# Kernel tuning notes

Measured on AMD Instinct MI355X. Metric: run time of the kernel, lower is better.

## Reference

```python
import jax, jax.numpy as jnp
import numpy as np

N = 100_000   # nodes
E = 1_600_000 # edges
D = 128       # hidden/input dim
OUT = 32      # output dim
G = 512       # graphs in batch
L = 3         # conv layers


def setup_inputs() -> dict:
    key = jax.random.key(0)
    ks = jax.random.split(key, 12)
    s = 1.0 / np.sqrt(D)
    inp = {
        "x": jax.random.normal(ks[0], (N, D), jnp.float32),
        "edge_index": jax.random.randint(ks[1], (2, E), 0, N, dtype=jnp.int32),
        "batch": jnp.sort(jax.random.randint(ks[2], (N,), 0, G, dtype=jnp.int32)),
        "enc_W1": jax.random.normal(ks[3], (D, D), jnp.float32) * s,
        "enc_b1": jnp.zeros((D,), jnp.float32),
        "enc_W2": jax.random.normal(ks[4], (D, D), jnp.float32) * s,
        "enc_b2": jnp.zeros((D,), jnp.float32),
        "gcn_W": jax.random.normal(ks[5], (L, D, D), jnp.float32) * s,
        "gcn_b": jnp.zeros((L, D), jnp.float32),
        "dec_W1": jax.random.normal(ks[6], (D, D), jnp.float32) * s,
        "dec_b1": jnp.zeros((D,), jnp.float32),
        "dec_W2": jax.random.normal(ks[7], (D, OUT), jnp.float32) * s,
        "dec_b2": jnp.zeros((OUT,), jnp.float32),
        "num_graphs": G,
    }
    return inp


def reference(x, edge_index, batch, enc_W1, enc_b1, enc_W2, enc_b2,
              gcn_W, gcn_b, dec_W1, dec_b1, dec_W2, dec_b2, num_graphs):
    n = x.shape[0]
    src, dst = edge_index[0], edge_index[1]

    # ---- encoder MLP (Linear -> ReLU -> Linear -> ReLU) ----
    h = jax.nn.relu(x @ enc_W1 + enc_b1)
    h = jax.nn.relu(h @ enc_W2 + enc_b2)

    # ---- GCN normalization: D^{-1/2} (A + I) D^{-1/2}, degrees incl. self-loops ----
    deg = jax.ops.segment_sum(jnp.ones_like(src, dtype=h.dtype), dst, num_segments=n) + 1.0
    inv_sqrt = jax.lax.rsqrt(deg)           # [N]
    edge_coef = inv_sqrt[src] * inv_sqrt[dst]  # [E]
    self_coef = inv_sqrt * inv_sqrt            # [N]

    # ---- GCN conv layers ----
    for l in range(gcn_W.shape[0]):
        hw = h @ gcn_W[l]                                       # [N, D]
        msgs = hw[src] * edge_coef[:, None]                     # [E, D] gather
        agg = jax.ops.segment_sum(msgs, dst, num_segments=n)    # [N, D] scatter-add
        agg = agg + hw * self_coef[:, None]                     # self loops
        h = jax.nn.relu(agg + gcn_b[l])

    # ---- global add pool over graphs ----
    pooled = jax.ops.segment_sum(h, batch, num_segments=num_graphs)  # [G, D]

    # ---- decoder MLP ----
    out = jax.nn.relu(pooled @ dec_W1 + dec_b1)
    return out @ dec_W2 + dec_b2
```

## Files before the change

kernel.cpp:

```cpp
#include <hip/hip_runtime.h>

#define NNODES 100000
#define NEDGES 1600000
#define DIM    128
#define OUTD   32
#define NGRAPH 512
#define LDA    136

#define NBUCK2  256
#define BSHIFT  9
#define CAP     12288
#define EPB2    8192
#define SBLOCKS ((NEDGES + EPB2 - 1) / EPB2)
#define NBUILD  ((NNODES + 511) / 512)
#define FBLOCKS ((NNODES + 127) / 128)

using bf16x8 = __attribute__((ext_vector_type(8))) short;
using f32x4  = __attribute__((ext_vector_type(4))) float;
using f32x2  = __attribute__((ext_vector_type(2))) float;

__device__ __forceinline__ short f2bf(float f) {
    unsigned u = __float_as_uint(f);
    unsigned r = (u + 0x7fff + ((u >> 16) & 1)) >> 16;
    return (short)r;
}
__device__ __forceinline__ float bf2f(short s) {
    return __uint_as_float(((unsigned)(unsigned short)s) << 16);
}
__device__ __forceinline__ float bf2f_lo(unsigned u) { return __uint_as_float(u << 16); }
__device__ __forceinline__ float bf2f_hi(unsigned u) { return __uint_as_float(u & 0xffff0000u); }

__device__ __forceinline__ uint2 bf8_to_fp8(bf16x8 t) {
    float f0 = bf2f(t[0]), f1 = bf2f(t[1]), f2 = bf2f(t[2]), f3 = bf2f(t[3]);
    float f4 = bf2f(t[4]), f5 = bf2f(t[5]), f6 = bf2f(t[6]), f7 = bf2f(t[7]);
    uint2 o;
    o.x = __builtin_amdgcn_cvt_pk_fp8_f32(f0, f1, 0, false);
    o.x = __builtin_amdgcn_cvt_pk_fp8_f32(f2, f3, o.x, true);
    o.y = __builtin_amdgcn_cvt_pk_fp8_f32(f4, f5, 0, false);
    o.y = __builtin_amdgcn_cvt_pk_fp8_f32(f6, f7, o.y, true);
    return o;
}

__global__ __launch_bounds__(256) void k_prep(
    const float* __restrict__ eW1, const float* __restrict__ eW2,
    const float* __restrict__ gW, short* __restrict__ WT,
    int* __restrict__ gcur, float* __restrict__ pooled)
{
    int idx = blockIdx.x * 256 + threadIdx.x;
    if (idx < 5 * 16384) {
        int mat = idx >> 14, rem = idx & 16383;
        int k = rem >> 7, n = rem & 127;
        const float* src = (mat == 0) ? eW1 : (mat == 1) ? eW2
                                            : (gW + (size_t)(mat - 2) * 16384);
        WT[(size_t)mat * 16384 + n * DIM + k] = f2bf(src[k * DIM + n]);
    }
    if (idx < NBUCK2) gcur[idx] = idx * CAP;
    if (idx < NGRAPH * DIM) pooled[idx] = 0.f;
}

__global__ __launch_bounds__(512) void k_scatter(
    const int* __restrict__ src, const int* __restrict__ dst,
    int* __restrict__ gcur, unsigned* __restrict__ tmp)
{
    __shared__ unsigned short rnk[EPB2];
    __shared__ int h[NBUCK2];
    __shared__ int gbase[NBUCK2];
    const int tid  = threadIdx.x;
    const int base = blockIdx.x * EPB2;
    if (tid < NBUCK2) h[tid] = 0;
    __syncthreads();
    #pragma unroll
    for (int it = 0; it < EPB2 / 512; ++it) {
        int e = base + it * 512 + tid;
        if (e < NEDGES) {
            int b = dst[e] >> BSHIFT;
            rnk[it * 512 + tid] = (unsigned short)atomicAdd(&h[b], 1);
        }
    }
    __syncthreads();
    if (tid < NBUCK2 && h[tid] > 0)
        gbase[tid] = atomicAdd(&gcur[tid], h[tid]);
    __syncthreads();
    #pragma unroll
    for (int it = 0; it < EPB2 / 512; ++it) {
        int e = base + it * 512 + tid;
        if (e < NEDGES) {
            int d = dst[e], sv = src[e];
            int b = d >> BSHIFT;
            int pos = gbase[b] + rnk[it * 512 + tid];
            if (pos < (b + 1) * CAP)
                tmp[pos] = (unsigned)sv | ((unsigned)(d & 511) << 17);
        }
    }
}

__global__ __launch_bounds__(512) void k_build(
    const unsigned* __restrict__ tmp, const int* __restrict__ gcur,
    int* __restrict__ row_off, int* __restrict__ cntA,
    float* __restrict__ inv, int* __restrict__ col)
{
    __shared__ int hist[512], sc[512], lcur[512];
    const int tid   = threadIdx.x;
    const int b     = blockIdx.x;
    const int tbase = b * CAP;
    const int cnt_b = min(gcur[b] - tbase, CAP);
    hist[tid] = 0;
    __syncthreads();
    for (int i = tid; i < cnt_b; i += 512)
        atomicAdd(&hist[(tmp[tbase + i] >> 17) & 511], 1);
    __syncthreads();
    const int hv = hist[tid];
    sc[tid] = hv;
    __syncthreads();
    for (int off = 1; off < 512; off <<= 1) {
        int t = (tid >= off) ? sc[tid - off] : 0;
        __syncthreads();
        sc[tid] += t;
        __syncthreads();
    }
    const int start = tbase + sc[tid] - hv;
    lcur[tid] = start;
    const int node = b * 512 + tid;
    if (node < NNODES) {
        row_off[node] = start;
        cntA[node]    = hv;
        inv[node]     = rsqrtf((float)hv + 1.0f);
    }
    __syncthreads();
    for (int i = tid; i < cnt_b; i += 512) {
        unsigned t = tmp[tbase + i];
        int pos = atomicAdd(&lcur[(t >> 17) & 511], 1);
        col[pos] = (int)(t & 0x1FFFFu);
    }
}

__global__ __launch_bounds__(512, 4) void k_enc(
    const float* __restrict__ x, const short* __restrict__ WT,
    const float* __restrict__ b1, const float* __restrict__ b2,
    const float* __restrict__ inv, unsigned char* __restrict__ g8, int M)
{
    __shared__ short As[128 * LDA];
    __shared__ short Bs[128 * LDA];

    const int tid = threadIdx.x;
    const int m0  = blockIdx.x * 128;

    #pragma unroll
    for (int i = 0; i < 4; ++i) {
        int u = tid + i * 512;
        int row = u >> 4, uc = (u & 15) << 3;
        int gr = min(m0 + row, M - 1);
        const float4* sp = (const float4*)(x + (size_t)gr * DIM + uc);
        float4 f0 = sp[0], f1 = sp[1];
        short t8[8] = { f2bf(f0.x), f2bf(f0.y), f2bf(f0.z), f2bf(f0.w),
                        f2bf(f1.x), f2bf(f1.y), f2bf(f1.z), f2bf(f1.w) };
        *(bf16x8*)&As[row * LDA + uc] = *(bf16x8*)t8;
    }

    const int wave = tid >> 6, lane = tid & 63;
    const int ml = lane & 15, quad = lane >> 4;
    const int w16 = wave * 16;

    #pragma unroll
    for (int mat = 0; mat < 3; ++mat) {
        if (mat > 0) __syncthreads();
        #pragma unroll
        for (int i = 0; i < 4; ++i) {
            int u = tid + i * 512;
            int n = u >> 4, kc = (u & 15) << 3;
            *(bf16x8*)&Bs[n * LDA + kc] =
                *(const bf16x8*)(WT + (size_t)mat * 16384 + n * DIM + kc);
        }
        __syncthreads();

        f32x4 acc[8] = {};
        #pragma unroll
        for (int kk = 0; kk < 4; ++kk) {
            const int k0 = kk * 32 + quad * 8;
            bf16x8 a = *(bf16x8*)&As[(w16 + ml) * LDA + k0];
            #pragma unroll
            for (int ni = 0; ni < 8; ++ni) {
                bf16x8 b = *(bf16x8*)&Bs[(ni * 16 + ml) * LDA + k0];
                acc[ni] = __builtin_amdgcn_mfma_f32_16x16x32_bf16(a, b, acc[ni], 0, 0, 0);
            }
        }
        #pragma unroll
        for (int ni = 0; ni < 8; ++ni) {
            const int colc = ni * 16 + ml;
            #pragma unroll
            for (int r = 0; r < 4; ++r) {
                const int rowl = w16 + quad * 4 + r;
                float v = acc[ni][r];
                if (mat == 0)      v = fmaxf(v + b1[colc], 0.f);
                else if (mat == 1) v = fmaxf(v + b2[colc], 0.f);
                else               v *= inv[min(m0 + rowl, M - 1)];
                As[rowl * LDA + colc] = f2bf(v);
            }
        }
    }
    __syncthreads();

    #pragma unroll
    for (int i = 0; i < 4; ++i) {
        int u = tid + i * 512;
        int row = u >> 4, uc = (u & 15) << 3;
        int gr = m0 + row;
        if (gr < M) {
            bf16x8 t = *(bf16x8*)&As[row * LDA + uc];
            *(uint2*)(g8 + (size_t)gr * DIM + uc) = bf8_to_fp8(t);
        }
    }
}

__global__ __launch_bounds__(256) void gemm_mfma(
    const short* __restrict__ A, const short* __restrict__ WT,
    const float* __restrict__ inv, unsigned char* __restrict__ g8, int M)
{
    __shared__ short As[128 * LDA];
    __shared__ short Bs[128 * LDA];

    const int tid = threadIdx.x;
    const int m0  = blockIdx.x * 128;

    #pragma unroll
    for (int i = 0; i < 8; ++i) {
        int idx = tid + i * 256;
        int row = idx >> 4, kg = (idx & 15) << 3;
        int r = min(m0 + row, M - 1);
        *(bf16x8*)&As[row * LDA + kg] = *(const bf16x8*)(A + (size_t)r * DIM + kg);
    }
    #pragma unroll
    for (int i = 0; i < 8; ++i) {
        int idx = tid + i * 256;
        int n = idx >> 4, kg = (idx & 15) << 3;
        *(bf16x8*)&Bs[n * LDA + kg] = *(const bf16x8*)(WT + n * DIM + kg);
    }
    __syncthreads();

    const int wave = tid >> 6, lane = tid & 63;
    const int ml = lane & 15, quad = lane >> 4;
    const int w32 = wave * 32;

    f32x4 acc[2][8] = {};
    #pragma unroll
    for (int kk = 0; kk < 4; ++kk) {
        const int k0 = kk * 32 + quad * 8;
        bf16x8 a0 = *(bf16x8*)&As[(w32 + ml) * LDA + k0];
        bf16x8 a1 = *(bf16x8*)&As[(w32 + 16 + ml) * LDA + k0];
        #pragma unroll
        for (int ni = 0; ni < 8; ++ni) {
            bf16x8 b = *(bf16x8*)&Bs[(ni * 16 + ml) * LDA + k0];
            acc[0][ni] = __builtin_amdgcn_mfma_f32_16x16x32_bf16(a0, b, acc[0][ni], 0, 0, 0);
            acc[1][ni] = __builtin_amdgcn_mfma_f32_16x16x32_bf16(a1, b, acc[1][ni], 0, 0, 0);
        }
    }
    __syncthreads();

    short* Cs = As;
    #pragma unroll
    for (int mi = 0; mi < 2; ++mi) {
        #pragma unroll
        for (int ni = 0; ni < 8; ++ni) {
            const int colc = ni * 16 + ml;
            #pragma unroll
            for (int r = 0; r < 4; ++r) {
                const int row = w32 + mi * 16 + quad * 4 + r;
                float v = acc[mi][ni][r] * inv[min(m0 + row, M - 1)];
                Cs[row * LDA + colc] = f2bf(v);
            }
        }
    }
    __syncthreads();
    #pragma unroll
    for (int i = 0; i < 8; ++i) {
        int idx = tid + i * 256;
        int row = idx >> 4, cg = (idx & 15) << 3;
        int gr = m0 + row;
        if (gr < M) {
            bf16x8 t = *(bf16x8*)&Cs[row * LDA + cg];
            *(uint2*)(g8 + (size_t)gr * DIM + cg) = bf8_to_fp8(t);
        }
    }
}

__global__ __launch_bounds__(512) void k_agg(
    const unsigned char* __restrict__ g8v, const int* __restrict__ row_off,
    const int* __restrict__ cntA, const int* __restrict__ col,
    const float* __restrict__ inv, const float* __restrict__ bias,
    short* __restrict__ hout)
{
    const int wid  = blockIdx.x * 8 + (threadIdx.x >> 6);
    const int lane = threadIdx.x & 63;
    const int q    = lane >> 4;
    const int sl   = lane & 15;
    const int node = wid * 4 + q;
    if (node >= NNODES) return;

    const uint2* hp = (const uint2*)g8v;
    uint2 us = hp[(size_t)node * 16 + sl];
    f32x2 p;
    float a0, a1, a2, a3, a4, a5, a6, a7;
    p = __builtin_amdgcn_cvt_pk_f32_fp8(us.x, false); a0 = p.x; a1 = p.y;
    p = __builtin_amdgcn_cvt_pk_f32_fp8(us.x, true);  a2 = p.x; a3 = p.y;
    p = __builtin_amdgcn_cvt_pk_f32_fp8(us.y, false); a4 = p.x; a5 = p.y;
    p = __builtin_amdgcn_cvt_pk_f32_fp8(us.y, true);  a6 = p.x; a7 = p.y;

    #define ACC8(v) \
        p = __builtin_amdgcn_cvt_pk_f32_fp8(v.x, false); a0 += p.x; a1 += p.y; \
        p = __builtin_amdgcn_cvt_pk_f32_fp8(v.x, true);  a2 += p.x; a3 += p.y; \
        p = __builtin_amdgcn_cvt_pk_f32_fp8(v.y, false); a4 += p.x; a5 += p.y; \
        p = __builtin_amdgcn_cvt_pk_f32_fp8(v.y, true);  a6 += p.x; a7 += p.y;

    const int s = row_off[node];
    const int e = s + cntA[node];
    int j = s;
    for (; j + 7 < e; j += 8) {
        uint2 v0 = hp[(size_t)col[j]     * 16 + sl];
        uint2 v1 = hp[(size_t)col[j + 1] * 16 + sl];
        uint2 v2 = hp[(size_t)col[j + 2] * 16 + sl];
        uint2 v3 = hp[(size_t)col[j + 3] * 16 + sl];
        uint2 v4 = hp[(size_t)col[j + 4] * 16 + sl];
        uint2 v5 = hp[(size_t)col[j + 5] * 16 + sl];
        uint2 v6 = hp[(size_t)col[j + 6] * 16 + sl];
        uint2 v7 = hp[(size_t)col[j + 7] * 16 + sl];
        ACC8(v0) ACC8(v1) ACC8(v2) ACC8(v3)
        ACC8(v4) ACC8(v5) ACC8(v6) ACC8(v7)
    }
    for (; j + 3 < e; j += 4) {
        uint2 v0 = hp[(size_t)col[j]     * 16 + sl];
        uint2 v1 = hp[(size_t)col[j + 1] * 16 + sl];
        uint2 v2 = hp[(size_t)col[j + 2] * 16 + sl];
        uint2 v3 = hp[(size_t)col[j + 3] * 16 + sl];
        ACC8(v0) ACC8(v1) ACC8(v2) ACC8(v3)
    }
    for (; j < e; ++j) {
        uint2 v = hp[(size_t)col[j] * 16 + sl];
        ACC8(v)
    }
    #undef ACC8

    const float scv = inv[node];
    const float4 bb0 = ((const float4*)bias)[sl * 2];
    const float4 bb1 = ((const float4*)bias)[sl * 2 + 1];
    short o[8];
    o[0] = f2bf(fmaxf(fmaf(a0, scv, bb0.x), 0.f));
    o[1] = f2bf(fmaxf(fmaf(a1, scv, bb0.y), 0.f));
    o[2] = f2bf(fmaxf(fmaf(a2, scv, bb0.z), 0.f));
    o[3] = f2bf(fmaxf(fmaf(a3, scv, bb0.w), 0.f));
    o[4] = f2bf(fmaxf(fmaf(a4, scv, bb1.x), 0.f));
    o[5] = f2bf(fmaxf(fmaf(a5, scv, bb1.y), 0.f));
    o[6] = f2bf(fmaxf(fmaf(a6, scv, bb1.z), 0.f));
    o[7] = f2bf(fmaxf(fmaf(a7, scv, bb1.w), 0.f));
    ((bf16x8*)hout)[(size_t)node * 16 + sl] = *(bf16x8*)o;
}

__global__ __launch_bounds__(512) void k_pool(
    const short* __restrict__ h, const int* __restrict__ batch,
    float* __restrict__ pooled)
{
    const int wave = threadIdx.x >> 6, lane = threadIdx.x & 63;
    const int node0 = blockIdx.x * 128 + wave * 16;
    const unsigned* hp = (const unsigned*)h;

    float gx = 0.f, gy = 0.f;
    int cg = -1;
    #pragma unroll 1
    for (int i = 0; i < 16; ++i) {
        const int node = node0 + i;
        if (node >= NNODES) break;
        const int g = batch[node];
        if (g != cg) {
            if (cg >= 0) {
                atomicAdd(pooled + (size_t)cg * DIM + lane * 2,     gx);
                atomicAdd(pooled + (size_t)cg * DIM + lane * 2 + 1, gy);
            }
            cg = g; gx = 0.f; gy = 0.f;
        }
        unsigned v = hp[(size_t)node * 64 + lane];
        gx += bf2f_lo(v);
        gy += bf2f_hi(v);
    }
    if (cg >= 0) {
        atomicAdd(pooled + (size_t)cg * DIM + lane * 2,     gx);
        atomicAdd(pooled + (size_t)cg * DIM + lane * 2 + 1, gy);
    }
}

__global__ __launch_bounds__(512) void k_dec(
    const float* __restrict__ pooled, const float* __restrict__ W1,
    const float* __restrict__ b1, const float* __restrict__ W2,
    const float* __restrict__ b2, float* __restrict__ out)
{
    __shared__ float pbuf[8][128];
    __shared__ float tbuf[8][128];
    const int wave = threadIdx.x >> 6, lane = threadIdx.x & 63;
    const int g = blockIdx.x * 8 + wave;

    float2 pv = *(const float2*)(pooled + (size_t)g * DIM + lane * 2);
    pbuf[wave][lane * 2]     = pv.x;
    pbuf[wave][lane * 2 + 1] = pv.y;
    __syncthreads();

    float t0 = 0.f, t1 = 0.f;
    #pragma unroll 8
    for (int k = 0; k < DIM; ++k) {
        float pk = pbuf[wave][k];
        float2 w = *(const float2*)(W1 + (size_t)k * DIM + lane * 2);
        t0 = fmaf(pk, w.x, t0);
        t1 = fmaf(pk, w.y, t1);
    }
    tbuf[wave][lane * 2]     = fmaxf(t0 + b1[lane * 2],     0.f);
    tbuf[wave][lane * 2 + 1] = fmaxf(t1 + b1[lane * 2 + 1], 0.f);
    __syncthreads();

    const int c = lane & 31, hh = lane >> 5;
    float part = 0.f;
    #pragma unroll 8
    for (int kk = 0; kk < 64; ++kk) {
        int k = hh * 64 + kk;
        part = fmaf(tbuf[wave][k], W2[(size_t)k * OUTD + c], part);
    }
    float other = __shfl_xor(part, 32, 64);
    if (hh == 0)
        out[(size_t)g * OUTD + c] = part + other + b2[c];
}

extern "C" void kernel_launch(void* const* d_in, const int* in_sizes, int n_in,
                              void* d_out, int out_size, void* d_ws, size_t ws_size,
                              hipStream_t stream)
{
    const float* x      = (const float*)d_in[0];
    const int*   ei     = (const int*)d_in[1];
    const int*   batch  = (const int*)d_in[2];
    const float* enc_W1 = (const float*)d_in[3];
    const float* enc_b1 = (const float*)d_in[4];
    const float* enc_W2 = (const float*)d_in[5];
    const float* enc_b2 = (const float*)d_in[6];
    const float* gcn_W  = (const float*)d_in[7];
    const float* gcn_b  = (const float*)d_in[8];
    const float* dec_W1 = (const float*)d_in[9];
    const float* dec_b1 = (const float*)d_in[10];
    const float* dec_W2 = (const float*)d_in[11];
    const float* dec_b2 = (const float*)d_in[12];
    float* out = (float*)d_out;

    const int* src = ei;
    const int* dst = ei + NEDGES;

    char* p = (char*)d_ws;
    auto alloc = [&](size_t bytes) -> void* {
        void* r = (void*)p;
        p += (bytes + 255) & ~(size_t)255;
        return r;
    };
    short*         hw     = (short*)        alloc((size_t)NNODES * DIM * sizeof(short));
    unsigned char* g8     = (unsigned char*)alloc((size_t)NNODES * DIM);
    float*         inv    = (float*)        alloc((size_t)NNODES * sizeof(float));
    int*           row_off= (int*)          alloc((size_t)NNODES * sizeof(int));
    int*           cntA   = (int*)          alloc((size_t)NNODES * sizeof(int));
    int*           col    = (int*)          alloc((size_t)NBUCK2 * CAP * sizeof(int));
    unsigned*      tmp    = (unsigned*)     alloc((size_t)NBUCK2 * CAP * sizeof(unsigned));
    int*           gcur   = (int*)          alloc((size_t)NBUCK2 * sizeof(int));
    short*         WT     = (short*)        alloc((size_t)5 * DIM * DIM * sizeof(short));
    float*         pooled = (float*)        alloc((size_t)NGRAPH * DIM * sizeof(float));

    k_prep   <<<(5 * 16384 + 255) / 256, 256, 0, stream>>>(enc_W1, enc_W2, gcn_W,
                                                           WT, gcur, pooled);
    k_scatter<<<SBLOCKS, 512, 0, stream>>>(src, dst, gcur, tmp);
    k_build  <<<NBUILD, 512, 0, stream>>>(tmp, gcur, row_off, cntA, inv, col);

    k_enc<<<FBLOCKS, 512, 0, stream>>>(x, WT, enc_b1, enc_b2, inv, g8, NNODES);

    const int aggBlocks = (NNODES + 31) / 32;
    k_agg<<<aggBlocks, 512, 0, stream>>>(g8, row_off, cntA, col, inv, gcn_b, hw);
    gemm_mfma<<<FBLOCKS, 256, 0, stream>>>(hw, WT + 3 * 16384, inv, g8, NNODES);
    k_agg<<<aggBlocks, 512, 0, stream>>>(g8, row_off, cntA, col, inv, gcn_b + 128, hw);
    gemm_mfma<<<FBLOCKS, 256, 0, stream>>>(hw, WT + 4 * 16384, inv, g8, NNODES);
    k_agg<<<aggBlocks, 512, 0, stream>>>(g8, row_off, cntA, col, inv, gcn_b + 256, hw);

    k_pool<<<FBLOCKS, 512, 0, stream>>>(hw, batch, pooled);
    k_dec <<<NGRAPH / 8, 512, 0, stream>>>(pooled, dec_W1, dec_b1,
                                           dec_W2, dec_b2, out);
}
```

Measured before the change: 334.9 us.

## Fuse GCN aggregation with next-layer GEMM and final aggregation with pooling

Aggregation for layers one and two now runs its MFMA transform to the next layer in the same kernel, with a 32-row tile per block. The bf16 hidden-state round trip through global memory and the separate GEMM launches are gone, and two fp8 buffers are ping-ponged. The last aggregation now sums into the graph pooling through shared memory, which replaces the separate pool kernel. In exchange each aggregation block reloads the full 128x128 weight tile, and the small per-block GEMM gives the MFMA units less work per wave.

```diff
diff --git a/kernel.cpp b/kernel.cpp
--- a/kernel.cpp
+++ b/kernel.cpp
@@ -14,6 +14,7 @@
 #define SBLOCKS ((NEDGES + EPB2 - 1) / EPB2)
 #define NBUILD  ((NNODES + 511) / 512)
 #define FBLOCKS ((NNODES + 127) / 128)
+#define AGGBLK  ((NNODES + 31) / 32)
 
 using bf16x8 = __attribute__((ext_vector_type(8))) short;
 using f32x4  = __attribute__((ext_vector_type(4))) float;
@@ -27,8 +28,6 @@
 __device__ __forceinline__ float bf2f(short s) {
     return __uint_as_float(((unsigned)(unsigned short)s) << 16);
 }
-__device__ __forceinline__ float bf2f_lo(unsigned u) { return __uint_as_float(u << 16); }
-__device__ __forceinline__ float bf2f_hi(unsigned u) { return __uint_as_float(u & 0xffff0000u); }
 
 __device__ __forceinline__ uint2 bf8_to_fp8(bf16x8 t) {
     float f0 = bf2f(t[0]), f1 = bf2f(t[1]), f2 = bf2f(t[2]), f3 = bf2f(t[3]);
@@ -212,89 +211,30 @@
     }
 }
 
-__global__ __launch_bounds__(256) void gemm_mfma(
-    const short* __restrict__ A, const short* __restrict__ WT,
-    const float* __restrict__ inv, unsigned char* __restrict__ g8, int M)
-{
-    __shared__ short As[128 * LDA];
-    __shared__ short Bs[128 * LDA];
-
-    const int tid = threadIdx.x;
-    const int m0  = blockIdx.x * 128;
-
-    #pragma unroll
-    for (int i = 0; i < 8; ++i) {
-        int idx = tid + i * 256;
-        int row = idx >> 4, kg = (idx & 15) << 3;
-        int r = min(m0 + row, M - 1);
-        *(bf16x8*)&As[row * LDA + kg] = *(const bf16x8*)(A + (size_t)r * DIM + kg);
-    }
-    #pragma unroll
-    for (int i = 0; i < 8; ++i) {
-        int idx = tid + i * 256;
-        int n = idx >> 4, kg = (idx & 15) << 3;
-        *(bf16x8*)&Bs[n * LDA + kg] = *(const bf16x8*)(WT + n * DIM + kg);
-    }
-    __syncthreads();
-
-    const int wave = tid >> 6, lane = tid & 63;
-    const int ml = lane & 15, quad = lane >> 4;
-    const int w32 = wave * 32;
-
-    f32x4 acc[2][8] = {};
-    #pragma unroll
-    for (int kk = 0; kk < 4; ++kk) {
-        const int k0 = kk * 32 + quad * 8;
-        bf16x8 a0 = *(bf16x8*)&As[(w32 + ml) * LDA + k0];
-        bf16x8 a1 = *(bf16x8*)&As[(w32 + 16 + ml) * LDA + k0];
-        #pragma unroll
-        for (int ni = 0; ni < 8; ++ni) {
-            bf16x8 b = *(bf16x8*)&Bs[(ni * 16 + ml) * LDA + k0];
-            acc[0][ni] = __builtin_amdgcn_mfma_f32_16x16x32_bf16(a0, b, acc[0][ni], 0, 0, 0);
-            acc[1][ni] = __builtin_amdgcn_mfma_f32_16x16x32_bf16(a1, b, acc[1][ni], 0, 0, 0);
-        }
-    }
-    __syncthreads();
-
-    short* Cs = As;
-    #pragma unroll
-    for (int mi = 0; mi < 2; ++mi) {
-        #pragma unroll
-        for (int ni = 0; ni < 8; ++ni) {
-            const int colc = ni * 16 + ml;
-            #pragma unroll
-            for (int r = 0; r < 4; ++r) {
-                const int row = w32 + mi * 16 + quad * 4 + r;
-                float v = acc[mi][ni][r] * inv[min(m0 + row, M - 1)];
-                Cs[row * LDA + colc] = f2bf(v);
-            }
-        }
-    }
-    __syncthreads();
-    #pragma unroll
-    for (int i = 0; i < 8; ++i) {
-        int idx = tid + i * 256;
-        int row = idx >> 4, cg = (idx & 15) << 3;
-        int gr = m0 + row;
-        if (gr < M) {
-            bf16x8 t = *(bf16x8*)&Cs[row * LDA + cg];
-            *(uint2*)(g8 + (size_t)gr * DIM + cg) = bf8_to_fp8(t);
-        }
-    }
-}
-
-__global__ __launch_bounds__(512) void k_agg(
+__global__ __launch_bounds__(512) void k_agg_gemm(
     const unsigned char* __restrict__ g8v, const int* __restrict__ row_off,
     const int* __restrict__ cntA, const int* __restrict__ col,
     const float* __restrict__ inv, const float* __restrict__ bias,
-    short* __restrict__ hout)
-{
-    const int wid  = blockIdx.x * 8 + (threadIdx.x >> 6);
-    const int lane = threadIdx.x & 63;
+    const short* __restrict__ WT, unsigned char* __restrict__ g8o)
+{
+    __shared__ short As[32 * LDA];
+    __shared__ short Bs[128 * LDA];
+
+    const int tid = threadIdx.x;
+
+    #pragma unroll
+    for (int i = 0; i < 4; ++i) {
+        int u = tid + i * 512;
+        int n = u >> 4, kc = (u & 15) << 3;
+        *(bf16x8*)&Bs[n * LDA + kc] = *(const bf16x8*)(WT + n * DIM + kc);
+    }
+
+    const int wave = tid >> 6, lane = tid & 63;
     const int q    = lane >> 4;
     const int sl   = lane & 15;
-    const int node = wid * 4 + q;
-    if (node >= NNODES) return;
+    const int nl   = wave * 4 + q;
+    const int m0   = blockIdx.x * 32;
+    const int node = m0 + nl;
 
     const uint2* hp = (const uint2*)g8v;
     uint2 us = hp[(size_t)node * 16 + sl];
@@ -351,39 +291,135 @@
     o[5] = f2bf(fmaxf(fmaf(a5, scv, bb1.y), 0.f));
     o[6] = f2bf(fmaxf(fmaf(a6, scv, bb1.z), 0.f));
     o[7] = f2bf(fmaxf(fmaf(a7, scv, bb1.w), 0.f));
-    ((bf16x8*)hout)[(size_t)node * 16 + sl] = *(bf16x8*)o;
-}
-
-__global__ __launch_bounds__(512) void k_pool(
-    const short* __restrict__ h, const int* __restrict__ batch,
-    float* __restrict__ pooled)
-{
-    const int wave = threadIdx.x >> 6, lane = threadIdx.x & 63;
-    const int node0 = blockIdx.x * 128 + wave * 16;
-    const unsigned* hp = (const unsigned*)h;
-
-    float gx = 0.f, gy = 0.f;
+    *(bf16x8*)&As[nl * LDA + sl * 8] = *(bf16x8*)o;
+    __syncthreads();
+
+    const int mh = wave >> 2;
+    const int nq = wave & 3;
+    f32x4 acc[2] = {};
+    #pragma unroll
+    for (int kk = 0; kk < 4; ++kk) {
+        const int k0 = kk * 32 + q * 8;
+        bf16x8 a = *(bf16x8*)&As[(mh * 16 + sl) * LDA + k0];
+        #pragma unroll
+        for (int ni = 0; ni < 2; ++ni) {
+            bf16x8 b = *(bf16x8*)&Bs[((nq * 2 + ni) * 16 + sl) * LDA + k0];
+            acc[ni] = __builtin_amdgcn_mfma_f32_16x16x32_bf16(a, b, acc[ni], 0, 0, 0);
+        }
+    }
+    __syncthreads();
+
+    #pragma unroll
+    for (int ni = 0; ni < 2; ++ni) {
+        const int colc = (nq * 2 + ni) * 16 + sl;
+        #pragma unroll
+        for (int r = 0; r < 4; ++r) {
+            const int rowl = mh * 16 + q * 4 + r;
+            As[rowl * LDA + colc] = f2bf(acc[ni][r] * inv[m0 + rowl]);
+        }
+    }
+    __syncthreads();
+
+    {
+        int row = tid >> 4, cg = (tid & 15) << 3;
+        bf16x8 t = *(bf16x8*)&As[row * LDA + cg];
+        *(uint2*)(g8o + (size_t)(m0 + row) * DIM + cg) = bf8_to_fp8(t);
+    }
+}
+
+__global__ __launch_bounds__(512) void k_agg_pool(
+    const unsigned char* __restrict__ g8v, const int* __restrict__ row_off,
+    const int* __restrict__ cntA, const int* __restrict__ col,
+    const float* __restrict__ inv, const float* __restrict__ bias,
+    const int* __restrict__ batch, float* __restrict__ pooled)
+{
+    __shared__ float Hs[32][132];
+    __shared__ int sbatch[32];
+
+    const int tid = threadIdx.x;
+    const int wave = tid >> 6, lane = tid & 63;
+    const int q    = lane >> 4;
+    const int sl   = lane & 15;
+    const int nl   = wave * 4 + q;
+    const int m0   = blockIdx.x * 32;
+    const int node = m0 + nl;
+
+    if (tid < 32) sbatch[tid] = batch[m0 + tid];
+
+    const uint2* hp = (const uint2*)g8v;
+    uint2 us = hp[(size_t)node * 16 + sl];
+    f32x2 p;
+    float a0, a1, a2, a3, a4, a5, a6, a7;
+    p = __builtin_amdgcn_cvt_pk_f32_fp8(us.x, false); a0 = p.x; a1 = p.y;
+    p = __builtin_amdgcn_cvt_pk_f32_fp8(us.x, true);  a2 = p.x; a3 = p.y;
+    p = __builtin_amdgcn_cvt_pk_f32_fp8(us.y, false); a4 = p.x; a5 = p.y;
+    p = __builtin_amdgcn_cvt_pk_f32_fp8(us.y, true);  a6 = p.x; a7 = p.y;
+
+    #define ACC8(v) \
+        p = __builtin_amdgcn_cvt_pk_f32_fp8(v.x, false); a0 += p.x; a1 += p.y; \
+        p = __builtin_amdgcn_cvt_pk_f32_fp8(v.x, true);  a2 += p.x; a3 += p.y; \
+        p = __builtin_amdgcn_cvt_pk_f32_fp8(v.y, false); a4 += p.x; a5 += p.y; \
+        p = __builtin_amdgcn_cvt_pk_f32_fp8(v.y, true);  a6 += p.x; a7 += p.y;
+
+    const int s = row_off[node];
+    const int e = s + cntA[node];
+    int j = s;
+    for (; j + 7 < e; j += 8) {
+        uint2 v0 = hp[(size_t)col[j]     * 16 + sl];
+        uint2 v1 = hp[(size_t)col[j + 1] * 16 + sl];
+        uint2 v2 = hp[(size_t)col[j + 2] * 16 + sl];
+        uint2 v3 = hp[(size_t)col[j + 3] * 16 + sl];
+        uint2 v4 = hp[(size_t)col[j + 4] * 16 + sl];
+        uint2 v5 = hp[(size_t)col[j + 5] * 16 + sl];
+        uint2 v6 = hp[(size_t)col[j + 6] * 16 + sl];
+        uint2 v7 = hp[(size_t)col[j + 7] * 16 + sl];
+        ACC8(v0) ACC8(v1) ACC8(v2) ACC8(v3)
+        ACC8(v4) ACC8(v5) ACC8(v6) ACC8(v7)
+    }
+    for (; j + 3 < e; j += 4) {
+        uint2 v0 = hp[(size_t)col[j]     * 16 + sl];
+        uint2 v1 = hp[(size_t)col[j + 1] * 16 + sl];
+        uint2 v2 = hp[(size_t)col[j + 2] * 16 + sl];
+        uint2 v3 = hp[(size_t)col[j + 3] * 16 + sl];
+        ACC8(v0) ACC8(v1) ACC8(v2) ACC8(v3)
+    }
+    for (; j < e; ++j) {
+        uint2 v = hp[(size_t)col[j] * 16 + sl];
+        ACC8(v)
+    }
+    #undef ACC8
+
+    const float scv = inv[node];
+    const float4 bb0 = ((const float4*)bias)[sl * 2];
+    const float4 bb1 = ((const float4*)bias)[sl * 2 + 1];
+    float4 h0, h1;
+    h0.x = fmaxf(fmaf(a0, scv, bb0.x), 0.f);
+    h0.y = fmaxf(fmaf(a1, scv, bb0.y), 0.f);
+    h0.z = fmaxf(fmaf(a2, scv, bb0.z), 0.f);
+    h0.w = fmaxf(fmaf(a3, scv, bb0.w), 0.f);
+    h1.x = fmaxf(fmaf(a4, scv, bb1.x), 0.f);
+    h1.y = fmaxf(fmaf(a5, scv, bb1.y), 0.f);
+    h1.z = fmaxf(fmaf(a6, scv, bb1.z), 0.f);
+    h1.w = fmaxf(fmaf(a7, scv, bb1.w), 0.f);
+    *(float4*)&Hs[nl][sl * 8]     = h0;
+    *(float4*)&Hs[nl][sl * 8 + 4] = h1;
+    __syncthreads();
+
+    const int d   = tid & 127;
+    const int grp = tid >> 7;
+    float acc = 0.f;
     int cg = -1;
-    #pragma unroll 1
-    for (int i = 0; i < 16; ++i) {
-        const int node = node0 + i;
-        if (node >= NNODES) break;
-        const int g = batch[node];
+    #pragma unroll
+    for (int i = 0; i < 8; ++i) {
+        const int nn = grp * 8 + i;
+        const int g  = sbatch[nn];
         if (g != cg) {
-            if (cg >= 0) {
-                atomicAdd(pooled + (size_t)cg * DIM + lane * 2,     gx);
-                atomicAdd(pooled + (size_t)cg * DIM + lane * 2 + 1, gy);
-            }
-            cg = g; gx = 0.f; gy = 0.f;
-        }
-        unsigned v = hp[(size_t)node * 64 + lane];
-        gx += bf2f_lo(v);
-        gy += bf2f_hi(v);
-    }
-    if (cg >= 0) {
-        atomicAdd(pooled + (size_t)cg * DIM + lane * 2,     gx);
-        atomicAdd(pooled + (size_t)cg * DIM + lane * 2 + 1, gy);
-    }
+            if (cg >= 0) atomicAdd(pooled + (size_t)cg * DIM + d, acc);
+            cg = g; acc = 0.f;
+        }
+        acc += Hs[nn][d];
+    }
+    atomicAdd(pooled + (size_t)cg * DIM + d, acc);
 }
 
 __global__ __launch_bounds__(512) void k_dec(
@@ -453,8 +489,8 @@
         p += (bytes + 255) & ~(size_t)255;
         return r;
     };
-    short*         hw     = (short*)        alloc((size_t)NNODES * DIM * sizeof(short));
-    unsigned char* g8     = (unsigned char*)alloc((size_t)NNODES * DIM);
+    unsigned char* g8a    = (unsigned char*)alloc((size_t)NNODES * DIM);
+    unsigned char* g8b    = (unsigned char*)alloc((size_t)NNODES * DIM);
     float*         inv    = (float*)        alloc((size_t)NNODES * sizeof(float));
     int*           row_off= (int*)          alloc((size_t)NNODES * sizeof(int));
     int*           cntA   = (int*)          alloc((size_t)NNODES * sizeof(int));
@@ -469,16 +505,15 @@
     k_scatter<<<SBLOCKS, 512, 0, stream>>>(src, dst, gcur, tmp);
     k_build  <<<NBUILD, 512, 0, stream>>>(tmp, gcur, row_off, cntA, inv, col);
 
-    k_enc<<<FBLOCKS, 512, 0, stream>>>(x, WT, enc_b1, enc_b2, inv, g8, NNODES);
-
-    const int aggBlocks = (NNODES + 31) / 32;
-    k_agg<<<aggBlocks, 512, 0, stream>>>(g8, row_off, cntA, col, inv, gcn_b, hw);
-    gemm_mfma<<<FBLOCKS, 256, 0, stream>>>(hw, WT + 3 * 16384, inv, g8, NNODES);
-    k_agg<<<aggBlocks, 512, 0, stream>>>(g8, row_off, cntA, col, inv, gcn_b + 128, hw);
-    gemm_mfma<<<FBLOCKS, 256, 0, stream>>>(hw, WT + 4 * 16384, inv, g8, NNODES);
-    k_agg<<<aggBlocks, 512, 0, stream>>>(g8, row_off, cntA, col, inv, gcn_b + 256, hw);
-
-    k_pool<<<FBLOCKS, 512, 0, stream>>>(hw, batch, pooled);
+    k_enc<<<FBLOCKS, 512, 0, stream>>>(x, WT, enc_b1, enc_b2, inv, g8a, NNODES);
+
+    k_agg_gemm<<<AGGBLK, 512, 0, stream>>>(g8a, row_off, cntA, col, inv,
+                                           gcn_b,       WT + 3 * 16384, g8b);
+    k_agg_gemm<<<AGGBLK, 512, 0, stream>>>(g8b, row_off, cntA, col, inv,
+                                           gcn_b + 128, WT + 4 * 16384, g8a);
+    k_agg_pool<<<AGGBLK, 512, 0, stream>>>(g8a, row_off, cntA, col, inv,
+                                           gcn_b + 256, batch, pooled);
+
     k_dec <<<NGRAPH / 8, 512, 0, stream>>>(pooled, dec_W1, dec_b1,
                                            dec_W2, dec_b2, out);
 }
```

Measured after the change: 303.8 us. 9.3% less time.
